# Kernel tuning notes

Measured on AMD Instinct MI355X. Metric: run time of the kernel, lower is better.

Reference implementation:

```python
import jax, jax.numpy as jnp
import numpy as np

B, TQ, TK, D, NA = 8, 512, 2048, 1024, 512
H, HD = 16, 64          # n_head, head_dim (D = H*HD)
NE, HID = 4, 32         # n_experts, expert hidden_dim
EPS = 1e-6


def _rmsnorm(x, w):
    return x * jax.lax.rsqrt(jnp.mean(x * x, axis=-1, keepdims=True) + EPS) * w


def setup_inputs() -> dict:
    key = jax.random.key(0)
    ks = jax.random.split(key, 20)
    r = lambda i, shp: jax.random.normal(ks[i], shp, dtype=jnp.float32) * 0.02
    return {
        'q': jax.random.normal(ks[0], (B, TQ, D), dtype=jnp.float32),
        'kv': jax.random.normal(ks[1], (B, TK, D), dtype=jnp.float32),
        'qn_w': jnp.ones((D,), jnp.float32),
        'kva_w': jnp.ones((D,), jnp.float32),
        'kvi_w': jnp.ones((D,), jnp.float32),
        'dn_w': jnp.ones((D,), jnp.float32),
        'fn_w': jnp.ones((D,), jnp.float32),
        'Wq': r(2, (D, D)), 'bq': jnp.zeros((D,), jnp.float32),
        'Wk': r(3, (D, D)), 'bk': jnp.zeros((D,), jnp.float32),
        'Wv': r(4, (D, D)), 'bv': jnp.zeros((D,), jnp.float32),
        'Wo': r(5, (D, D)), 'bo': jnp.zeros((D,), jnp.float32),
        'active_bias': r(6, (D,)),
        'inactive_bias': r(7, (D,)),
        'log_temp': jnp.array(0.0, jnp.float32),
        'gate_attn': jnp.array(0.3, jnp.float32),
        'gate_ffn': jnp.array(0.7, jnp.float32),
        'Wr': r(8, (D, NE)), 'br': jnp.zeros((NE,), jnp.float32),
        'W1': r(9, (NE, D, 2 * HID)), 'b1': jnp.zeros((NE, 2 * HID), jnp.float32),
        'W2': r(10, (NE, HID, D)), 'b2': jnp.zeros((NE, D), jnp.float32),
        'kv_mask': jnp.ones((B, TK), bool),
        'n_actives': NA,
    }


def _forward(q, kv, qn_w, kva_w, kvi_w, dn_w, fn_w,
             Wq, bq, Wk, bk, Wv, bv, Wo, bo,
             active_bias, inactive_bias, log_temp, gate_attn, gate_ffn,
             Wr, br, W1, b1, W2, b2, kv_mask, n_actives):
    Na = int(n_actives)
    Tk = kv.shape[1]
    Ni = Tk - Na
    b, tq, d = q.shape

    # split-normed kv, with active/inactive learned biases injected pre-KV-proj
    kv_a = _rmsnorm(kv[:, :Na], kva_w) + active_bias
    kv_i = _rmsnorm(kv[:, Na:], kvi_w) + inactive_bias
    kv_b = jnp.concatenate([kv_a, kv_i], axis=1)

    qn = _rmsnorm(q, qn_w)
    qp = (qn @ Wq + bq).reshape(b, tq, H, HD).transpose(0, 2, 1, 3)  # (B,H,Tq,hd)
    k = (kv_b @ Wk + bk).reshape(b, Tk, H, HD).transpose(0, 2, 1, 3)
    v = (kv_b @ Wv + bv).reshape(b, Tk, H, HD).transpose(0, 2, 1, 3)

    # torch: q *= 1/sqrt(hd), then SDPA(q/temp, ...) applies another 1/sqrt(hd)
    temp = jnp.clip(jnp.exp(log_temp), 0.1, 10.0)
    scale = 1.0 / (HD * temp)

    def attn(kk, vv):
        logits = jnp.einsum('bhqd,bhkd->bhqk', qp, kk) * scale
        return jnp.einsum('bhqk,bhkd->bhqd', jax.nn.softmax(logits, axis=-1), vv)

    out = attn(k[:, :, :Na], v[:, :, :Na]) / np.sqrt(max(Na, 1)) \
        - attn(k[:, :, Na:], v[:, :, Na:]) / np.sqrt(max(Ni, 1))
    out = out.transpose(0, 2, 1, 3).reshape(b, tq, d)
    delta = _rmsnorm(out @ Wo + bo, dn_w)
    q_new = q + jax.nn.sigmoid(gate_attn) * delta

    # dense soft MoE over normed kv, with query-similarity logit bias
    x = _rmsnorm(kv, fn_w)
    logits = x @ Wr + br                                   # (B,Tk,NE)
    q_vec = jnp.mean(q_new, axis=1, keepdims=True)         # (B,1,D)
    sim = jnp.einsum('bqd,btd->bt', q_vec, x)              # (B,Tk)
    probs = jax.nn.softmax(logits + sim[..., None], axis=-1)

    h = jnp.einsum('btd,edh->bteh', x, W1) + b1            # (B,Tk,NE,2*HID)
    xp, g = h[..., :HID], h[..., HID:]
    act = xp * (g * jax.nn.sigmoid(g))                     # SwiGLU
    eo = jnp.einsum('bteh,ehd->bted', act, W2) + b2        # (B,Tk,NE,D)
    moe_out = jnp.einsum('bte,bted->btd', probs, eo)

    kv_new = kv + jax.nn.sigmoid(gate_ffn) * moe_out
    return q_new, kv_new


def reference(q, kv, qn_w, kva_w, kvi_w, dn_w, fn_w,
              Wq, bq, Wk, bk, Wv, bv, Wo, bo,
              active_bias, inactive_bias, log_temp, gate_attn, gate_ffn,
              Wr, br, W1, b1, W2, b2, kv_mask, n_actives):
    return _forward(q, kv, qn_w, kva_w, kvi_w, dn_w, fn_w,
                    Wq, bq, Wk, bk, Wv, bv, Wo, bo,
                    active_bias, inactive_bias, log_temp, gate_attn, gate_ffn,
                    Wr, br, W1, b1, W2, b2, kv_mask, n_actives)
```

## Files before the change

### kernel.cpp

```cpp
#include <hip/hip_runtime.h>
#include <hip/hip_bf16.h>
#include <stdint.h>


#define B_   8
#define TQ_  512
#define TK_  2048
#define D_   1024
#define H_   16
#define HD_  64
#define NE_  4
#define HID_ 32
#define EPSF 1e-6f
#define LOG2E 1.44269504f

typedef __bf16 bf16_t;
typedef __bf16 bf16x8 __attribute__((ext_vector_type(8)));
typedef __bf16 bf16x4 __attribute__((ext_vector_type(4)));
typedef float  f32x4  __attribute__((ext_vector_type(4)));

typedef __attribute__((address_space(1))) void gvoid_t;
typedef __attribute__((address_space(3))) void lvoid_t;

__device__ __forceinline__ void gld_lds16(const void* g, void* l) {
  __builtin_amdgcn_global_load_lds((gvoid_t*)g, (lvoid_t*)l, 16, 0, 0);
}

struct TP4 { const float* in[4]; bf16_t* out[4]; };

__global__ void transpose_conv4_kernel(TP4 p) {
  __shared__ float tile[32][33];
  const int bz = blockIdx.z;
  const float* in = p.in[bz];
  bf16_t* out = p.out[bz];
  const int rb = blockIdx.y * 32, cb = blockIdx.x * 32;
  const int txi = threadIdx.x, tyi = threadIdx.y;
#pragma unroll
  for (int i = 0; i < 32; i += 8)
    tile[tyi + i][txi] = in[(size_t)(rb + tyi + i) * D_ + cb + txi];
  __syncthreads();
#pragma unroll
  for (int i = 0; i < 32; i += 8)
    out[(size_t)(cb + tyi + i) * D_ + rb + txi] = (bf16_t)tile[txi][tyi + i];
}

__global__ void transpose_conv_kernel(const float* __restrict__ in, bf16_t* __restrict__ out,
                                      int R, int C, int in_bstride,
                                      int out_rstride, int ob_row, int ob_col) {
  __shared__ float tile[32][33];
  const int bz = blockIdx.z;
  const int rb = blockIdx.y * 32, cb = blockIdx.x * 32;
  const int txi = threadIdx.x, tyi = threadIdx.y;
  const float* inp = in + (size_t)bz * in_bstride;
#pragma unroll
  for (int i = 0; i < 32; i += 8) {
    const int r = rb + tyi + i, c = cb + txi;
    if (r < R && c < C) tile[tyi + i][txi] = inp[(size_t)r * C + c];
  }
  __syncthreads();
#pragma unroll
  for (int i = 0; i < 32; i += 8) {
    const int orow = cb + tyi + i;
    const int ocol = rb + txi;
    if (orow < C && ocol < R)
      out[(size_t)(orow + bz * ob_row) * out_rstride + bz * ob_col + ocol] =
          (bf16_t)tile[txi][tyi + i];
  }
}

__device__ __forceinline__ float block_rsum(float v, float* red) {
  v += __shfl_xor(v, 1);  v += __shfl_xor(v, 2);  v += __shfl_xor(v, 4);
  v += __shfl_xor(v, 8);  v += __shfl_xor(v, 16); v += __shfl_xor(v, 32);
  const int tid = threadIdx.x;
  if ((tid & 63) == 0) red[tid >> 6] = v;
  __syncthreads();
  return red[0] + red[1] + red[2] + red[3];
}

__global__ __launch_bounds__(256)
void rms_kv_kernel(const float* __restrict__ kv, const float* __restrict__ kva_w,
                   const float* __restrict__ kvi_w, const float* __restrict__ fn_w,
                   const float* __restrict__ ab, const float* __restrict__ ib,
                   const int* __restrict__ n_act, const float* __restrict__ Wr,
                   const float* __restrict__ br,
                   bf16_t* __restrict__ kvb, bf16_t* __restrict__ xn,
                   float* __restrict__ probs) {
  __shared__ float red[4];
  __shared__ f32x4 pred[4];
  const int row = blockIdx.x;
  const int t = row & (TK_ - 1);
  const int tid = threadIdx.x;
  const float* src = kv + (size_t)row * D_;
  f32x4 v = ((const f32x4*)src)[tid];
  float ss = v[0]*v[0] + v[1]*v[1] + v[2]*v[2] + v[3]*v[3];
  ss = block_rsum(ss, red);
  const float rs = rsqrtf(ss * (1.0f / D_) + EPSF);
  const int Na = n_act[0];
  const float* wsel = (t < Na) ? kva_w : kvi_w;
  const float* bsel = (t < Na) ? ab : ib;
  const int d = tid * 4;
  f32x4 wv = *(const f32x4*)(wsel + d);
  f32x4 bv = *(const f32x4*)(bsel + d);
  f32x4 fv = *(const f32x4*)(fn_w + d);
  bf16x4 o0, o1;
  f32x4 p4 = {};
#pragma unroll
  for (int c = 0; c < 4; ++c) {
    const float xv = v[c] * rs;
    const float xf = xv * fv[c];
    o0[c] = (bf16_t)(xv * wv[c] + bv[c]);
    o1[c] = (bf16_t)xf;
    const f32x4 w4 = *(const f32x4*)&Wr[(d + c) * 4];
    p4 += w4 * xf;
  }
  *(bf16x4*)&kvb[(size_t)row * D_ + d] = o0;
  *(bf16x4*)&xn [(size_t)row * D_ + d] = o1;
#pragma unroll
  for (int m = 1; m <= 32; m <<= 1) {
    p4[0] += __shfl_xor(p4[0], m); p4[1] += __shfl_xor(p4[1], m);
    p4[2] += __shfl_xor(p4[2], m); p4[3] += __shfl_xor(p4[3], m);
  }
  if ((tid & 63) == 0) pred[tid >> 6] = p4;
  __syncthreads();
  if (tid == 0) {
    f32x4 s = pred[0] + pred[1] + pred[2] + pred[3];
    s[0] += br[0]; s[1] += br[1]; s[2] += br[2]; s[3] += br[3];
    const float mx = fmaxf(fmaxf(s[0], s[1]), fmaxf(s[2], s[3]));
    const float e0 = __expf(s[0] - mx), e1 = __expf(s[1] - mx);
    const float e2 = __expf(s[2] - mx), e3 = __expf(s[3] - mx);
    const float inv = 1.0f / (e0 + e1 + e2 + e3);
    f32x4 pr = { e0 * inv, e1 * inv, e2 * inv, e3 * inv };
    *(f32x4*)&probs[row * 4] = pr;
  }
}

__global__ __launch_bounds__(256)
void rms_q_kernel(const float* __restrict__ q, const float* __restrict__ qn_w,
                  bf16_t* __restrict__ qn) {
  __shared__ float red[4];
  const int row = blockIdx.x;
  const int tid = threadIdx.x;
  const float* src = q + (size_t)row * D_;
  f32x4 v = ((const f32x4*)src)[tid];
  float ss = v[0]*v[0] + v[1]*v[1] + v[2]*v[2] + v[3]*v[3];
  ss = block_rsum(ss, red);
  const float rs = rsqrtf(ss * (1.0f / D_) + EPSF);
  const int d = tid * 4;
  f32x4 wv = *(const f32x4*)(qn_w + d);
  bf16x4 o0;
#pragma unroll
  for (int c = 0; c < 4; ++c) o0[c] = (bf16_t)(v[c] * rs * wv[c]);
  *(bf16x4*)&qn[(size_t)row * D_ + d] = o0;
}

__device__ __forceinline__ int xcd_swz(int bx, int gx) {
  if ((gx & 7) == 0) { const int cpx = gx >> 3; return (bx & 7) * cpx + (bx >> 3); }
  return bx;
}

__device__ __forceinline__ void gemm_loop_db(const bf16_t* __restrict__ ga,
                                             const bf16_t* __restrict__ gb,
                                             bf16_t* As, bf16_t* Bs, int K,
                                             size_t rstep, int ar, int br2,
                                             int tid, f32x4 acc[4][4]) {
  gld_lds16(ga,         &As[tid * 8]);
  gld_lds16(ga + rstep, &As[2048 + tid * 8]);
  gld_lds16(gb,         &Bs[tid * 8]);
  gld_lds16(gb + rstep, &Bs[2048 + tid * 8]);
  int buf = 0;
  for (int k0 = 0; k0 < K; k0 += 32) {
    __syncthreads();
    if (k0 + 32 < K) {
      const int nb = buf ^ 1;
      gld_lds16(ga + k0 + 32,         &As[nb * 4096 + tid * 8]);
      gld_lds16(ga + k0 + 32 + rstep, &As[nb * 4096 + 2048 + tid * 8]);
      gld_lds16(gb + k0 + 32,         &Bs[nb * 4096 + tid * 8]);
      gld_lds16(gb + k0 + 32 + rstep, &Bs[nb * 4096 + 2048 + tid * 8]);
    }
    bf16x8 af[4], bfr[4];
#pragma unroll
    for (int i = 0; i < 4; ++i) af[i]  = *(const bf16x8*)&As[buf * 4096 + ar  + i * 512];
#pragma unroll
    for (int j = 0; j < 4; ++j) bfr[j] = *(const bf16x8*)&Bs[buf * 4096 + br2 + j * 512];
#pragma unroll
    for (int i = 0; i < 4; ++i)
#pragma unroll
      for (int j = 0; j < 4; ++j)
        acc[i][j] = __builtin_amdgcn_mfma_f32_16x16x32_bf16(af[i], bfr[j], acc[i][j], 0, 0, 0);
    buf ^= 1;
  }
}

__device__ __forceinline__ void gemm64_loop_db(const bf16_t* __restrict__ ga,
                                               const bf16_t* __restrict__ gb,
                                               bf16_t* As, bf16_t* Bs, int K,
                                               size_t rstep, int ar, int br2,
                                               int tid, f32x4 acc[2][4]) {
  gld_lds16(ga,         &As[tid * 8]);
  gld_lds16(gb,         &Bs[tid * 8]);
  gld_lds16(gb + rstep, &Bs[2048 + tid * 8]);
  int buf = 0;
  for (int k0 = 0; k0 < K; k0 += 32) {
    __syncthreads();
    if (k0 + 32 < K) {
      const int nb = buf ^ 1;
      gld_lds16(ga + k0 + 32,         &As[nb * 2048 + tid * 8]);
      gld_lds16(gb + k0 + 32,         &Bs[nb * 4096 + tid * 8]);
      gld_lds16(gb + k0 + 32 + rstep, &Bs[nb * 4096 + 2048 + tid * 8]);
    }
    bf16x8 af[2], bfr[4];
#pragma unroll
    for (int i = 0; i < 2; ++i) af[i]  = *(const bf16x8*)&As[buf * 2048 + ar  + i * 512];
#pragma unroll
    for (int j = 0; j < 4; ++j) bfr[j] = *(const bf16x8*)&Bs[buf * 4096 + br2 + j * 512];
#pragma unroll
    for (int i = 0; i < 2; ++i)
#pragma unroll
      for (int j = 0; j < 4; ++j)
        acc[i][j] = __builtin_amdgcn_mfma_f32_16x16x32_bf16(af[i], bfr[j], acc[i][j], 0, 0, 0);
    buf ^= 1;
  }
}

template<int HAS_BIAS>
__global__ __launch_bounds__(256)
void gemm_tn(const bf16_t* __restrict__ A, const bf16_t* __restrict__ Wt,
             const float* __restrict__ bias, bf16_t* __restrict__ C,
             int M, int N, int K) {
  __shared__ alignas(16) bf16_t As[2 * 128 * 32];
  __shared__ alignas(16) bf16_t Bs[2 * 128 * 32];
  const int tid = threadIdx.x;
  const int lane = tid & 63;
  const int w = tid >> 6;
  const int wr = w >> 1, wc = w & 1;
  const int m0 = xcd_swz(blockIdx.x, gridDim.x) * 128;
  const int n0 = blockIdx.y * 128;

  f32x4 acc[4][4] = {};
  const bf16_t* ga = A  + (size_t)(m0 + (tid >> 2)) * K + (tid & 3) * 8;
  const bf16_t* gb = Wt + (size_t)(n0 + (tid >> 2)) * K + (tid & 3) * 8;
  const int kb = (lane >> 4) * 8;
  const int ar  = ((wr * 64 + (lane & 15)) << 5) + kb;
  const int br2 = ((wc * 64 + (lane & 15)) << 5) + kb;

  gemm_loop_db(ga, gb, As, Bs, K, (size_t)64 * K, ar, br2, tid, acc);

  const int row0 = m0 + wr * 64 + ((lane >> 4) << 2);
  const int col0 = n0 + wc * 64 + (lane & 15);
#pragma unroll
  for (int j = 0; j < 4; ++j) {
    const int cc = col0 + j * 16;
    const float bv = HAS_BIAS ? bias[cc] : 0.0f;
#pragma unroll
    for (int i = 0; i < 4; ++i) {
      const int rr = row0 + i * 16;
#pragma unroll
      for (int r = 0; r < 4; ++r)
        C[(size_t)(rr + r) * N + cc] = (bf16_t)(acc[i][j][r] + bv);
    }
  }
}

template<int HAS_BIAS>
__global__ __launch_bounds__(256)
void gemm64_tn(const bf16_t* __restrict__ A, const bf16_t* __restrict__ Wt,
               const float* __restrict__ bias, bf16_t* __restrict__ C,
               int M, int N, int K) {
  __shared__ alignas(16) bf16_t As[2 * 64 * 32];
  __shared__ alignas(16) bf16_t Bs[2 * 128 * 32];
  const int tid = threadIdx.x;
  const int lane = tid & 63;
  const int w = tid >> 6;
  const int wr = w >> 1, wc = w & 1;
  const int m0 = xcd_swz(blockIdx.x, gridDim.x) * 64;
  const int n0 = blockIdx.y * 128;

  f32x4 acc[2][4] = {};
  const bf16_t* ga = A  + (size_t)(m0 + (tid >> 2)) * K + (tid & 3) * 8;
  const bf16_t* gb = Wt + (size_t)(n0 + (tid >> 2)) * K + (tid & 3) * 8;
  const int kb = (lane >> 4) * 8;
  const int ar  = ((wr * 32 + (lane & 15)) << 5) + kb;
  const int br2 = ((wc * 64 + (lane & 15)) << 5) + kb;

  gemm64_loop_db(ga, gb, As, Bs, K, (size_t)64 * K, ar, br2, tid, acc);

  const int row0 = m0 + wr * 32 + ((lane >> 4) << 2);
  const int col0 = n0 + wc * 64 + (lane & 15);
#pragma unroll
  for (int j = 0; j < 4; ++j) {
    const int cc = col0 + j * 16;
    const float bv = HAS_BIAS ? bias[cc] : 0.0f;
#pragma unroll
    for (int i = 0; i < 2; ++i) {
      const int rr = row0 + i * 16;
#pragma unroll
      for (int r = 0; r < 4; ++r)
        C[(size_t)(rr + r) * N + cc] = (bf16_t)(acc[i][j][r] + bv);
    }
  }
}

__global__ __launch_bounds__(256)
void gemm_vt(const bf16_t* __restrict__ A, const bf16_t* __restrict__ Wt0,
             const float* __restrict__ bias, bf16_t* __restrict__ C0) {
  __shared__ alignas(16) bf16_t As[2 * 128 * 32];
  __shared__ alignas(16) bf16_t Bs[2 * 128 * 32];
  const int K = D_, N = TK_;
  const bf16_t* Wt = Wt0 + (size_t)blockIdx.z * TK_ * D_;
  bf16_t* C = C0 + (size_t)blockIdx.z * D_ * TK_;
  const int tid = threadIdx.x;
  const int lane = tid & 63;
  const int w = tid >> 6;
  const int wr = w >> 1, wc = w & 1;
  const int m0 = blockIdx.x * 128;
  const int n0 = blockIdx.y * 128;

  f32x4 acc[4][4] = {};
  const bf16_t* ga = A  + (size_t)(m0 + (tid >> 2)) * K + (tid & 3) * 8;
  const bf16_t* gb = Wt + (size_t)(n0 + (tid >> 2)) * K + (tid & 3) * 8;
  const int kb = (lane >> 4) * 8;
  const int ar  = ((wr * 64 + (lane & 15)) << 5) + kb;
  const int br2 = ((wc * 64 + (lane & 15)) << 5) + kb;

  gemm_loop_db(ga, gb, As, Bs, K, (size_t)64 * K, ar, br2, tid, acc);

  const int row0 = m0 + wr * 64 + ((lane >> 4) << 2);
  const int col0 = n0 + wc * 64 + (lane & 15);
#pragma unroll
  for (int i = 0; i < 4; ++i) {
    const int rr = row0 + i * 16;
#pragma unroll
    for (int r = 0; r < 4; ++r) {
      const float bv = bias[rr + r];
#pragma unroll
      for (int j = 0; j < 4; ++j)
        C[(size_t)(rr + r) * N + col0 + j * 16] = (bf16_t)(acc[i][j][r] + bv);
    }
  }
}

__global__ __launch_bounds__(256)
void gemm64_h_act(const bf16_t* __restrict__ A, const bf16_t* __restrict__ Wt,
                  const float* __restrict__ bias, const float* __restrict__ probs,
                  bf16_t* __restrict__ a2) {
  __shared__ alignas(16) bf16_t As[2 * 64 * 32];
  __shared__ alignas(16) bf16_t Bs[2 * 128 * 32];
  const int K = D_;
  const int tid = threadIdx.x;
  const int lane = tid & 63;
  const int w = tid >> 6;
  const int wr = w >> 1, wc = w & 1;
  const int m0 = xcd_swz(blockIdx.x, gridDim.x) * 64;
  const int n0 = blockIdx.y * 128;

  f32x4 acc[2][4] = {};
  const bf16_t* ga = A  + (size_t)(m0 + (tid >> 2)) * K + (tid & 3) * 8;
  const bf16_t* gb = Wt + (size_t)(n0 + (tid >> 2)) * K + (tid & 3) * 8;
  const int kb = (lane >> 4) * 8;
  const int ar  = ((wr * 32 + (lane & 15)) << 5) + kb;
  const int br2 = ((wc * 64 + (lane & 15)) << 5) + kb;

  gemm64_loop_db(ga, gb, As, Bs, K, (size_t)64 * K, ar, br2, tid, acc);

  const int row0 = m0 + wr * 32 + ((lane >> 4) << 2);
  const int hbase = n0 + wc * 64 + (lane & 15);
  const int e = hbase >> 6;
#pragma unroll
  for (int j = 0; j < 2; ++j) {
    const int ch = hbase + j * 16;
    const float bx = bias[ch], bg = bias[ch + 32];
    const int ac = (ch & 63) + e * 32;
#pragma unroll
    for (int i = 0; i < 2; ++i) {
      const int rr = row0 + i * 16;
#pragma unroll
      for (int r = 0; r < 4; ++r) {
        const float xp = acc[i][j][r] + bx;
        const float g  = acc[i][j + 2][r] + bg;
        const float sg = 1.0f / (1.0f + __expf(-g));
        const float pr = probs[(size_t)(rr + r) * 4 + e];
        a2[(size_t)(rr + r) * 128 + ac] = (bf16_t)(pr * xp * g * sg);
      }
    }
  }
}

__global__ __launch_bounds__(256)
void gemm_moe_kvnew(const bf16_t* __restrict__ A, const bf16_t* __restrict__ Wt,
                    const float* __restrict__ kv, const float* __restrict__ probs,
                    const float* __restrict__ b2, const float* __restrict__ gate_ffn,
                    float* __restrict__ out) {
  __shared__ alignas(16) bf16_t As[2 * 128 * 32];
  __shared__ alignas(16) bf16_t Bs[2 * 128 * 32];
  const int K = 128, N = D_;
  const int tid = threadIdx.x;
  const int lane = tid & 63;
  const int w = tid >> 6;
  const int wr = w >> 1, wc = w & 1;
  const int m0 = xcd_swz(blockIdx.x, gridDim.x) * 128;
  const int n0 = blockIdx.y * 128;

  f32x4 acc[4][4] = {};
  const bf16_t* ga = A  + (size_t)(m0 + (tid >> 2)) * K + (tid & 3) * 8;
  const bf16_t* gb = Wt + (size_t)(n0 + (tid >> 2)) * K + (tid & 3) * 8;
  const int kb = (lane >> 4) * 8;
  const int ar  = ((wr * 64 + (lane & 15)) << 5) + kb;
  const int br2 = ((wc * 64 + (lane & 15)) << 5) + kb;

  gemm_loop_db(ga, gb, As, Bs, K, (size_t)64 * K, ar, br2, tid, acc);

  const float sgf = 1.0f / (1.0f + __expf(-gate_ffn[0]));
  const int row0 = m0 + wr * 64 + ((lane >> 4) << 2);
  const int col0 = n0 + wc * 64 + (lane & 15);
#pragma unroll
  for (int j = 0; j < 4; ++j) {
    const int cc = col0 + j * 16;
    const f32x4 b2v = { b2[0 * D_ + cc], b2[1 * D_ + cc], b2[2 * D_ + cc], b2[3 * D_ + cc] };
#pragma unroll
    for (int i = 0; i < 4; ++i) {
      const int rr = row0 + i * 16;
#pragma unroll
      for (int r = 0; r < 4; ++r) {
        const f32x4 pr = *(const f32x4*)&probs[(size_t)(rr + r) * 4];
        const float bsum = pr[0]*b2v[0] + pr[1]*b2v[1] + pr[2]*b2v[2] + pr[3]*b2v[3];
        out[(size_t)(rr + r) * N + cc] =
            kv[(size_t)(rr + r) * N + cc] + sgf * (acc[i][j][r] + bsum);
      }
    }
  }
}

__global__ __launch_bounds__(256, 3)
void attn_mfma_kernel(const bf16_t* __restrict__ qp, const bf16_t* __restrict__ kb,
                      const bf16_t* __restrict__ vt, bf16_t* __restrict__ attno,
                      const float* __restrict__ log_temp, const int* __restrict__ n_act) {
  __shared__ alignas(16) bf16_t Ks[2][64 * 64];
  __shared__ alignas(16) bf16_t Vs[2][64 * 64];
  __shared__ alignas(16) bf16_t Ps[4][32 * 64];

  const int dd = blockIdx.x;
  const int xcd = dd & 7, within = dd >> 3;
  const int qt = within & 3, slot0 = within >> 2;
  const int bh = slot0 * 8 + xcd;
  const int b = bh >> 4, h = bh & 15;

  const int tid = threadIdx.x;
  const int lane = tid & 63;
  const int w = tid >> 6;
  const int lane15 = lane & 15, lgrp = lane >> 4, l7 = lane & 7;
  const int Na = n_act[0];
  float temp = __expf(log_temp[0]);
  temp = fminf(fmaxf(temp, 0.1f), 10.0f);
  const float lsc = LOG2E / (64.0f * temp);
  const int rowbase = qt * 128 + w * 32;

  const bf16_t* qsrcA = qp + (size_t)(b * TQ_ + rowbase + lane15) * D_ + h * 64 + lgrp * 8;
  const bf16_t* qsrcB = qsrcA + (size_t)16 * D_;
  bf16x8 qfA0 = *(const bf16x8*)qsrcA;
  bf16x8 qfA1 = *(const bf16x8*)(qsrcA + 32);
  bf16x8 qfB0 = *(const bf16x8*)qsrcB;
  bf16x8 qfB1 = *(const bf16x8*)(qsrcB + 32);
#pragma unroll
  for (int j = 0; j < 8; ++j) {
    qfA0[j] = (bf16_t)((float)qfA0[j] * lsc);
    qfA1[j] = (bf16_t)((float)qfA1[j] * lsc);
    qfB0[j] = (bf16_t)((float)qfB0[j] * lsc);
    qfB1[j] = (bf16_t)((float)qfB1[j] * lsc);
  }

  const int srow = tid >> 3;
  const int schunk = (tid & 7) ^ (srow & 7);
  const bf16_t* ksrc = kb + (size_t)(b * TK_ + srow) * D_ + h * 64 + schunk * 8;
  const bf16_t* vsrc = vt + ((size_t)(b * 16 + h) * 64 + srow) * TK_ + schunk * 8;

  f32x4 oA[4] = {}, oB[4] = {}, outA[4] = {}, outB[4] = {};
  float laccA = 0.f, laccB = 0.f;

  const float inv_sa = rsqrtf((float)(Na > 1 ? Na : 1));
  const int Ni = TK_ - Na;
  const float inv_si = rsqrtf((float)(Ni > 1 ? Ni : 1));

  gld_lds16(ksrc,            &Ks[0][tid * 8]);
  gld_lds16(ksrc + 32 * D_,  &Ks[0][2048 + tid * 8]);
  gld_lds16(vsrc,            &Vs[0][tid * 8]);
  gld_lds16(vsrc + 32 * TK_, &Vs[0][2048 + tid * 8]);

  for (int t = 0; t < TK_ / 64; ++t) {
    const int cur = t & 1;
    __syncthreads();
    if (t + 1 < TK_ / 64) {
      const int nb = cur ^ 1;
      const bf16_t* kN = ksrc + (size_t)(t + 1) * 64 * D_;
      const bf16_t* vN = vsrc + (size_t)(t + 1) * 64;
      gld_lds16(kN,            &Ks[nb][tid * 8]);
      gld_lds16(kN + 32 * D_,  &Ks[nb][2048 + tid * 8]);
      gld_lds16(vN,            &Vs[nb][tid * 8]);
      gld_lds16(vN + 32 * TK_, &Vs[nb][2048 + tid * 8]);
    }

    f32x4 sA[4], sB[4];
    __builtin_amdgcn_s_setprio(1);
#pragma unroll
    for (int cf = 0; cf < 4; ++cf) {
      const int krow = (cf * 16 + lane15) * 64;
      const bf16x8 kf0 = *(const bf16x8*)&Ks[cur][krow + ((lgrp ^ l7) << 3)];
      const bf16x8 kf1 = *(const bf16x8*)&Ks[cur][krow + (((lgrp + 4) ^ l7) << 3)];
      f32x4 s = {};
      s = __builtin_amdgcn_mfma_f32_16x16x32_bf16(kf0, qfA0, s, 0, 0, 0);
      s = __builtin_amdgcn_mfma_f32_16x16x32_bf16(kf1, qfA1, s, 0, 0, 0);
      sA[cf] = s;
      f32x4 s2 = {};
      s2 = __builtin_amdgcn_mfma_f32_16x16x32_bf16(kf0, qfB0, s2, 0, 0, 0);
      s2 = __builtin_amdgcn_mfma_f32_16x16x32_bf16(kf1, qfB1, s2, 0, 0, 0);
      sB[cf] = s2;
    }
    __builtin_amdgcn_s_setprio(0);

#pragma unroll
    for (int cf = 0; cf < 4; ++cf) {
      const int c = cf * 2 + (lgrp >> 1);
      const int pcol = ((c ^ l7) << 3) + (lgrp & 1) * 4;
      f32x4 pA, pB;
#pragma unroll
      for (int r = 0; r < 4; ++r) pA[r] = exp2f(sA[cf][r]);
#pragma unroll
      for (int r = 0; r < 4; ++r) pB[r] = exp2f(sB[cf][r]);
      laccA += (pA[0] + pA[1]) + (pA[2] + pA[3]);
      laccB += (pB[0] + pB[1]) + (pB[2] + pB[3]);
      bf16x4 pvA, pvB;
#pragma unroll
      for (int r = 0; r < 4; ++r) { pvA[r] = (bf16_t)pA[r]; pvB[r] = (bf16_t)pB[r]; }
      *(bf16x4*)&Ps[w][lane15 * 64 + pcol]        = pvA;
      *(bf16x4*)&Ps[w][(16 + lane15) * 64 + pcol] = pvB;
    }

    {
      const int prowA = lane15 * 64;
      const int prowB = (16 + lane15) * 64;
      const bf16x8 paA0 = *(const bf16x8*)&Ps[w][prowA + ((lgrp ^ l7) << 3)];
      const bf16x8 paA1 = *(const bf16x8*)&Ps[w][prowA + (((lgrp + 4) ^ l7) << 3)];
      const bf16x8 paB0 = *(const bf16x8*)&Ps[w][prowB + ((lgrp ^ l7) << 3)];
      const bf16x8 paB1 = *(const bf16x8*)&Ps[w][prowB + (((lgrp + 4) ^ l7) << 3)];
      __builtin_amdgcn_s_setprio(1);
#pragma unroll
      for (int df = 0; df < 4; ++df) {
        const int vrow = (df * 16 + lane15) * 64;
        const bf16x8 vf0 = *(const bf16x8*)&Vs[cur][vrow + ((lgrp ^ l7) << 3)];
        const bf16x8 vf1 = *(const bf16x8*)&Vs[cur][vrow + (((lgrp + 4) ^ l7) << 3)];
        oA[df] = __builtin_amdgcn_mfma_f32_16x16x32_bf16(paA0, vf0, oA[df], 0, 0, 0);
        oA[df] = __builtin_amdgcn_mfma_f32_16x16x32_bf16(paA1, vf1, oA[df], 0, 0, 0);
        oB[df] = __builtin_amdgcn_mfma_f32_16x16x32_bf16(paB0, vf0, oB[df], 0, 0, 0);
        oB[df] = __builtin_amdgcn_mfma_f32_16x16x32_bf16(paB1, vf1, oB[df], 0, 0, 0);
      }
      __builtin_amdgcn_s_setprio(0);
    }

    const bool endA = ((t + 1) * 64 == Na);
    const bool endI = (t == TK_ / 64 - 1);
    if (endA || endI) {
      float lA = laccA, lB = laccB;
      lA += __shfl_xor(lA, 16); lA += __shfl_xor(lA, 32);
      lB += __shfl_xor(lB, 16); lB += __shfl_xor(lB, 32);
      const float ssc = endA ? inv_sa : -inv_si;
      f32x4 ivA, ivB;
#pragma unroll
      for (int r = 0; r < 4; ++r) {
        ivA[r] = ssc / __shfl(lA, lgrp * 4 + r);
        ivB[r] = ssc / __shfl(lB, lgrp * 4 + r);
      }
#pragma unroll
      for (int df = 0; df < 4; ++df) {
        outA[df] += oA[df] * ivA; oA[df] = (f32x4){};
        outB[df] += oB[df] * ivB; oB[df] = (f32x4){};
      }
      laccA = 0.f; laccB = 0.f;
    }
  }

#pragma unroll
  for (int df = 0; df < 4; ++df)
#pragma unroll
    for (int r = 0; r < 4; ++r) {
      const size_t ro = (size_t)(b * TQ_ + rowbase + lgrp * 4 + r) * D_ + h * 64 + df * 16 + lane15;
      attno[ro]             = (bf16_t)outA[df][r];
      attno[ro + 16 * D_]   = (bf16_t)outB[df][r];
    }
}

__global__ __launch_bounds__(256)
void delta_qnew_kernel(const bf16_t* __restrict__ proj, const float* __restrict__ dn_w,
                       const float* __restrict__ q, const float* __restrict__ gate_attn,
                       float* __restrict__ qnew) {
  __shared__ float red[4];
  const int row = blockIdx.x;
  const int tid = threadIdx.x;
  bf16x4 pv = *(const bf16x4*)(proj + (size_t)row * D_ + tid * 4);
  f32x4 v;
#pragma unroll
  for (int c = 0; c < 4; ++c) v[c] = (float)pv[c];
  float ss = v[0]*v[0] + v[1]*v[1] + v[2]*v[2] + v[3]*v[3];
  ss = block_rsum(ss, red);
  const float rs = rsqrtf(ss * (1.0f / D_) + EPSF);
  const float sga = 1.0f / (1.0f + __expf(-gate_attn[0]));
  const int d = tid * 4;
  f32x4 wv = *(const f32x4*)(dn_w + d);
  f32x4 qv = *(const f32x4*)(q + (size_t)row * D_ + d);
  f32x4 out;
#pragma unroll
  for (int c = 0; c < 4; ++c) out[c] = qv[c] + sga * (v[c] * rs * wv[c]);
  *(f32x4*)&qnew[(size_t)row * D_ + d] = out;
}

extern "C" void kernel_launch(void* const* d_in, const int* in_sizes, int n_in,
                              void* d_out, int out_size, void* d_ws, size_t ws_size,
                              hipStream_t stream) {
  const float* q           = (const float*)d_in[0];
  const float* kv          = (const float*)d_in[1];
  const float* qn_w        = (const float*)d_in[2];
  const float* kva_w       = (const float*)d_in[3];
  const float* kvi_w       = (const float*)d_in[4];
  const float* dn_w        = (const float*)d_in[5];
  const float* fn_w        = (const float*)d_in[6];
  const float* Wq          = (const float*)d_in[7];
  const float* bq          = (const float*)d_in[8];
  const float* Wk          = (const float*)d_in[9];
  const float* bk          = (const float*)d_in[10];
  const float* Wv          = (const float*)d_in[11];
  const float* bv          = (const float*)d_in[12];
  const float* Wo          = (const float*)d_in[13];
  const float* bo          = (const float*)d_in[14];
  const float* active_bias = (const float*)d_in[15];
  const float* inactive_b  = (const float*)d_in[16];
  const float* log_temp    = (const float*)d_in[17];
  const float* gate_attn   = (const float*)d_in[18];
  const float* gate_ffn    = (const float*)d_in[19];
  const float* Wr          = (const float*)d_in[20];
  const float* br          = (const float*)d_in[21];
  const float* W1          = (const float*)d_in[22];
  const float* b1          = (const float*)d_in[23];
  const float* W2          = (const float*)d_in[24];
  const float* b2          = (const float*)d_in[25];
  const int*   n_act       = (const int*)d_in[27];

  char* ws = (char*)d_ws;
  size_t off = 0;
  auto alloc = [&](size_t bytes) -> char* {
    char* p = ws + off;
    off = (off + bytes + 255) & ~(size_t)255;
    return p;
  };

  bf16_t* wqT  = (bf16_t*)alloc((size_t)D_ * D_ * 2);
  bf16_t* wkT  = (bf16_t*)alloc((size_t)D_ * D_ * 2);
  bf16_t* wvT  = (bf16_t*)alloc((size_t)D_ * D_ * 2);
  bf16_t* woT  = (bf16_t*)alloc((size_t)D_ * D_ * 2);
  bf16_t* w1T  = (bf16_t*)alloc((size_t)256 * D_ * 2);
  bf16_t* w2T  = (bf16_t*)alloc((size_t)D_ * 128 * 2);
  bf16_t* kvb  = (bf16_t*)alloc((size_t)B_ * TK_ * D_ * 2);
  bf16_t* xn   = (bf16_t*)alloc((size_t)B_ * TK_ * D_ * 2);
  bf16_t* qn   = (bf16_t*)alloc((size_t)B_ * TQ_ * D_ * 2);
  bf16_t* qp   = (bf16_t*)alloc((size_t)B_ * TQ_ * D_ * 2);
  bf16_t* kbuf = (bf16_t*)alloc((size_t)B_ * TK_ * D_ * 2);
  bf16_t* vt   = (bf16_t*)alloc((size_t)B_ * D_ * TK_ * 2);
  float*  probs = (float*)alloc((size_t)B_ * TK_ * NE_ * 4);
  bf16_t* attno = qn;
  bf16_t* proj  = qp;
  bf16_t* a2buf = kbuf;
  (void)ws_size; (void)in_sizes; (void)n_in; (void)out_size;

  float* q_new_out  = (float*)d_out;
  float* kv_new_out = (float*)d_out + (size_t)B_ * TQ_ * D_;

  dim3 tb(32, 8);
  TP4 tp;
  tp.in[0] = Wq; tp.in[1] = Wk; tp.in[2] = Wv; tp.in[3] = Wo;
  tp.out[0] = wqT; tp.out[1] = wkT; tp.out[2] = wvT; tp.out[3] = woT;
  transpose_conv4_kernel<<<dim3(32, 32, 4), tb, 0, stream>>>(tp);
  transpose_conv_kernel<<<dim3(2, 32, 4), tb, 0, stream>>>(W1, w1T, D_, 64, D_ * 64, D_, 64, 0);
  transpose_conv_kernel<<<dim3(32, 1, 4), tb, 0, stream>>>(W2, w2T, 32, D_, 32 * D_, 128, 0, 32);

  rms_kv_kernel<<<B_ * TK_, 256, 0, stream>>>(kv, kva_w, kvi_w, fn_w, active_bias,
                                              inactive_b, n_act, Wr, br, kvb, xn, probs);
  rms_q_kernel<<<B_ * TQ_, 256, 0, stream>>>(q, qn_w, qn);

  gemm64_tn<1><<<dim3(B_ * TQ_ / 64, D_ / 128), 256, 0, stream>>>(qn, wqT, bq, qp, B_ * TQ_, D_, D_);
  gemm_tn<1><<<dim3(B_ * TK_ / 128, D_ / 128), 256, 0, stream>>>(kvb, wkT, bk, kbuf, B_ * TK_, D_, D_);
  gemm_vt<<<dim3(D_ / 128, TK_ / 128, B_), 256, 0, stream>>>(wvT, kvb, bv, vt);

  attn_mfma_kernel<<<B_ * H_ * (TQ_ / 128), 256, 0, stream>>>(qp, kbuf, vt, attno, log_temp, n_act);

  gemm64_tn<1><<<dim3(B_ * TQ_ / 64, D_ / 128), 256, 0, stream>>>(attno, woT, bo, proj, B_ * TQ_, D_, D_);
  delta_qnew_kernel<<<B_ * TQ_, 256, 0, stream>>>(proj, dn_w, q, gate_attn, q_new_out);

  gemm64_h_act<<<dim3(B_ * TK_ / 64, 2), 256, 0, stream>>>(xn, w1T, b1, probs, a2buf);
  gemm_moe_kvnew<<<dim3(B_ * TK_ / 128, D_ / 128), 256, 0, stream>>>(a2buf, w2T, kv, probs, b2,
                                                                     gate_ffn, kv_new_out);
}
```

Baseline: 339.4 us.

## Fuse K and V projections into one GEMM and halve attention block size

Merges the K projection and the transposed V projection into a single kernel that loads each kv tile once and drives two MFMA accumulator sets. The V result is transposed through LDS so it can be written to the Vt layout with coalesced stores. This removes one launch and one full read of the normalized kv activations, at the cost of more accumulator registers and extra LDS traffic in the epilogue. The attention kernel is also reconfigured to 128-thread blocks covering 64 query rows, which doubles the grid and changes the K/V tile loading pattern.

```diff
diff --git a/kernel.cpp b/kernel.cpp
--- a/kernel.cpp
+++ b/kernel.cpp
@@ -156,6 +156,111 @@
 __device__ __forceinline__ int xcd_swz(int bx, int gx) {
   if ((gx & 7) == 0) { const int cpx = gx >> 3; return (bx & 7) * cpx + (bx >> 3); }
   return bx;
+}
+
+__global__ __launch_bounds__(256)
+void gemm_kv(const bf16_t* __restrict__ A, const bf16_t* __restrict__ Wk,
+             const bf16_t* __restrict__ Wv, const float* __restrict__ bk,
+             const float* __restrict__ bv, bf16_t* __restrict__ Kout,
+             bf16_t* __restrict__ Vt) {
+  __shared__ alignas(16) bf16_t lds[3 * 8192];
+  bf16_t* As  = lds;
+  bf16_t* Bks = lds + 8192;
+  bf16_t* Bvs = lds + 16384;
+  const int K = D_;
+  const int tid = threadIdx.x;
+  const int lane = tid & 63;
+  const int w = tid >> 6;
+  const int wr = w >> 1, wc = w & 1;
+  const int lane15 = lane & 15, lgrp = lane >> 4;
+  const int m0 = xcd_swz(blockIdx.x, gridDim.x) * 128;
+  const int n0 = blockIdx.y * 128;
+
+  f32x4 acc_k[4][4] = {};
+  f32x4 acc_v[4][4] = {};
+
+  const bf16_t* ga = A  + (size_t)(m0 + (tid >> 2)) * K + (tid & 3) * 8;
+  const bf16_t* gk = Wk + (size_t)(n0 + (tid >> 2)) * K + (tid & 3) * 8;
+  const bf16_t* gv = Wv + (size_t)(n0 + (tid >> 2)) * K + (tid & 3) * 8;
+  const size_t rstep = (size_t)64 * K;
+  const int kb = lgrp * 8;
+  const int ar  = ((wr * 64 + lane15) << 5) + kb;
+  const int br2 = ((wc * 64 + lane15) << 5) + kb;
+
+  gld_lds16(ga,         &As[tid * 8]);
+  gld_lds16(ga + rstep, &As[2048 + tid * 8]);
+  gld_lds16(gk,         &Bks[tid * 8]);
+  gld_lds16(gk + rstep, &Bks[2048 + tid * 8]);
+  gld_lds16(gv,         &Bvs[tid * 8]);
+  gld_lds16(gv + rstep, &Bvs[2048 + tid * 8]);
+  int buf = 0;
+  for (int k0 = 0; k0 < K; k0 += 32) {
+    __syncthreads();
+    if (k0 + 32 < K) {
+      const int nb = buf ^ 1;
+      gld_lds16(ga + k0 + 32,         &As[nb * 4096 + tid * 8]);
+      gld_lds16(ga + k0 + 32 + rstep, &As[nb * 4096 + 2048 + tid * 8]);
+      gld_lds16(gk + k0 + 32,         &Bks[nb * 4096 + tid * 8]);
+      gld_lds16(gk + k0 + 32 + rstep, &Bks[nb * 4096 + 2048 + tid * 8]);
+      gld_lds16(gv + k0 + 32,         &Bvs[nb * 4096 + tid * 8]);
+      gld_lds16(gv + k0 + 32 + rstep, &Bvs[nb * 4096 + 2048 + tid * 8]);
+    }
+    bf16x8 af[4], bkf[4], bvf[4];
+#pragma unroll
+    for (int i = 0; i < 4; ++i) af[i]  = *(const bf16x8*)&As [buf * 4096 + ar  + i * 512];
+#pragma unroll
+    for (int j = 0; j < 4; ++j) bkf[j] = *(const bf16x8*)&Bks[buf * 4096 + br2 + j * 512];
+#pragma unroll
+    for (int j = 0; j < 4; ++j) bvf[j] = *(const bf16x8*)&Bvs[buf * 4096 + br2 + j * 512];
+    __builtin_amdgcn_s_setprio(1);
+#pragma unroll
+    for (int i = 0; i < 4; ++i)
+#pragma unroll
+      for (int j = 0; j < 4; ++j) {
+        acc_k[i][j] = __builtin_amdgcn_mfma_f32_16x16x32_bf16(af[i], bkf[j], acc_k[i][j], 0, 0, 0);
+        acc_v[i][j] = __builtin_amdgcn_mfma_f32_16x16x32_bf16(af[i], bvf[j], acc_v[i][j], 0, 0, 0);
+      }
+    __builtin_amdgcn_s_setprio(0);
+    buf ^= 1;
+  }
+
+  const int row0 = m0 + wr * 64 + (lgrp << 2);
+  const int col0 = n0 + wc * 64 + lane15;
+#pragma unroll
+  for (int j = 0; j < 4; ++j) {
+    const int cc = col0 + j * 16;
+    const float bkv = bk[cc];
+#pragma unroll
+    for (int i = 0; i < 4; ++i) {
+      const int rr = row0 + i * 16;
+#pragma unroll
+      for (int r = 0; r < 4; ++r)
+        Kout[(size_t)(rr + r) * D_ + cc] = (bf16_t)(acc_k[i][j][r] + bkv);
+    }
+  }
+
+  __syncthreads();
+  bf16_t* vt_l = lds + w * 4608;
+#pragma unroll
+  for (int j = 0; j < 4; ++j) {
+    const int nl = j * 16 + lane15;
+    const float bvv = bv[n0 + wc * 64 + nl];
+#pragma unroll
+    for (int i = 0; i < 4; ++i)
+#pragma unroll
+      for (int r = 0; r < 4; ++r)
+        vt_l[nl * 72 + i * 16 + lgrp * 4 + r] = (bf16_t)(acc_v[i][j][r] + bvv);
+  }
+  const int bidx2 = m0 >> 11;
+  const int tok0 = (m0 & (TK_ - 1)) + wr * 64;
+  bf16_t* vbase = Vt + (size_t)bidx2 * D_ * TK_ + (size_t)(n0 + wc * 64) * TK_ + tok0;
+#pragma unroll
+  for (int it = 0; it < 8; ++it) {
+    const int ln = (lane >> 3) + it * 8;
+    const int tk = (lane & 7) * 8;
+    const bf16x8 v8 = *(const bf16x8*)&vt_l[ln * 72 + tk];
+    *(bf16x8*)&vbase[(size_t)ln * TK_ + tk] = v8;
+  }
 }
 
 __device__ __forceinline__ void gemm_loop_db(const bf16_t* __restrict__ ga,
@@ -224,45 +329,6 @@
 
 template<int HAS_BIAS>
 __global__ __launch_bounds__(256)
-void gemm_tn(const bf16_t* __restrict__ A, const bf16_t* __restrict__ Wt,
-             const float* __restrict__ bias, bf16_t* __restrict__ C,
-             int M, int N, int K) {
-  __shared__ alignas(16) bf16_t As[2 * 128 * 32];
-  __shared__ alignas(16) bf16_t Bs[2 * 128 * 32];
-  const int tid = threadIdx.x;
-  const int lane = tid & 63;
-  const int w = tid >> 6;
-  const int wr = w >> 1, wc = w & 1;
-  const int m0 = xcd_swz(blockIdx.x, gridDim.x) * 128;
-  const int n0 = blockIdx.y * 128;
-
-  f32x4 acc[4][4] = {};
-  const bf16_t* ga = A  + (size_t)(m0 + (tid >> 2)) * K + (tid & 3) * 8;
-  const bf16_t* gb = Wt + (size_t)(n0 + (tid >> 2)) * K + (tid & 3) * 8;
-  const int kb = (lane >> 4) * 8;
-  const int ar  = ((wr * 64 + (lane & 15)) << 5) + kb;
-  const int br2 = ((wc * 64 + (lane & 15)) << 5) + kb;
-
-  gemm_loop_db(ga, gb, As, Bs, K, (size_t)64 * K, ar, br2, tid, acc);
-
-  const int row0 = m0 + wr * 64 + ((lane >> 4) << 2);
-  const int col0 = n0 + wc * 64 + (lane & 15);
-#pragma unroll
-  for (int j = 0; j < 4; ++j) {
-    const int cc = col0 + j * 16;
-    const float bv = HAS_BIAS ? bias[cc] : 0.0f;
-#pragma unroll
-    for (int i = 0; i < 4; ++i) {
-      const int rr = row0 + i * 16;
-#pragma unroll
-      for (int r = 0; r < 4; ++r)
-        C[(size_t)(rr + r) * N + cc] = (bf16_t)(acc[i][j][r] + bv);
-    }
-  }
-}
-
-template<int HAS_BIAS>
-__global__ __launch_bounds__(256)
 void gemm64_tn(const bf16_t* __restrict__ A, const bf16_t* __restrict__ Wt,
                const float* __restrict__ bias, bf16_t* __restrict__ C,
                int M, int N, int K) {
@@ -296,45 +362,6 @@
 #pragma unroll
       for (int r = 0; r < 4; ++r)
         C[(size_t)(rr + r) * N + cc] = (bf16_t)(acc[i][j][r] + bv);
-    }
-  }
-}
-
-__global__ __launch_bounds__(256)
-void gemm_vt(const bf16_t* __restrict__ A, const bf16_t* __restrict__ Wt0,
-             const float* __restrict__ bias, bf16_t* __restrict__ C0) {
-  __shared__ alignas(16) bf16_t As[2 * 128 * 32];
-  __shared__ alignas(16) bf16_t Bs[2 * 128 * 32];
-  const int K = D_, N = TK_;
-  const bf16_t* Wt = Wt0 + (size_t)blockIdx.z * TK_ * D_;
-  bf16_t* C = C0 + (size_t)blockIdx.z * D_ * TK_;
-  const int tid = threadIdx.x;
-  const int lane = tid & 63;
-  const int w = tid >> 6;
-  const int wr = w >> 1, wc = w & 1;
-  const int m0 = blockIdx.x * 128;
-  const int n0 = blockIdx.y * 128;
-
-  f32x4 acc[4][4] = {};
-  const bf16_t* ga = A  + (size_t)(m0 + (tid >> 2)) * K + (tid & 3) * 8;
-  const bf16_t* gb = Wt + (size_t)(n0 + (tid >> 2)) * K + (tid & 3) * 8;
-  const int kb = (lane >> 4) * 8;
-  const int ar  = ((wr * 64 + (lane & 15)) << 5) + kb;
-  const int br2 = ((wc * 64 + (lane & 15)) << 5) + kb;
-
-  gemm_loop_db(ga, gb, As, Bs, K, (size_t)64 * K, ar, br2, tid, acc);
-
-  const int row0 = m0 + wr * 64 + ((lane >> 4) << 2);
-  const int col0 = n0 + wc * 64 + (lane & 15);
-#pragma unroll
-  for (int i = 0; i < 4; ++i) {
-    const int rr = row0 + i * 16;
-#pragma unroll
-    for (int r = 0; r < 4; ++r) {
-      const float bv = bias[rr + r];
-#pragma unroll
-      for (int j = 0; j < 4; ++j)
-        C[(size_t)(rr + r) * N + col0 + j * 16] = (bf16_t)(acc[i][j][r] + bv);
     }
   }
 }
@@ -430,17 +457,17 @@
   }
 }
 
-__global__ __launch_bounds__(256, 3)
+__global__ __launch_bounds__(128, 2)
 void attn_mfma_kernel(const bf16_t* __restrict__ qp, const bf16_t* __restrict__ kb,
                       const bf16_t* __restrict__ vt, bf16_t* __restrict__ attno,
                       const float* __restrict__ log_temp, const int* __restrict__ n_act) {
   __shared__ alignas(16) bf16_t Ks[2][64 * 64];
   __shared__ alignas(16) bf16_t Vs[2][64 * 64];
-  __shared__ alignas(16) bf16_t Ps[4][32 * 64];
+  __shared__ alignas(16) bf16_t Ps[2][32 * 64];
 
   const int dd = blockIdx.x;
   const int xcd = dd & 7, within = dd >> 3;
-  const int qt = within & 3, slot0 = within >> 2;
+  const int qt = within & 7, slot0 = within >> 3;
   const int bh = slot0 * 8 + xcd;
   const int b = bh >> 4, h = bh & 15;
 
@@ -452,7 +479,7 @@
   float temp = __expf(log_temp[0]);
   temp = fminf(fmaxf(temp, 0.1f), 10.0f);
   const float lsc = LOG2E / (64.0f * temp);
-  const int rowbase = qt * 128 + w * 32;
+  const int rowbase = qt * 64 + w * 32;
 
   const bf16_t* qsrcA = qp + (size_t)(b * TQ_ + rowbase + lane15) * D_ + h * 64 + lgrp * 8;
   const bf16_t* qsrcB = qsrcA + (size_t)16 * D_;
@@ -480,10 +507,11 @@
   const int Ni = TK_ - Na;
   const float inv_si = rsqrtf((float)(Ni > 1 ? Ni : 1));
 
-  gld_lds16(ksrc,            &Ks[0][tid * 8]);
-  gld_lds16(ksrc + 32 * D_,  &Ks[0][2048 + tid * 8]);
-  gld_lds16(vsrc,            &Vs[0][tid * 8]);
-  gld_lds16(vsrc + 32 * TK_, &Vs[0][2048 + tid * 8]);
+#pragma unroll
+  for (int r = 0; r < 4; ++r) {
+    gld_lds16(ksrc + (size_t)r * 16 * D_, &Ks[0][r * 1024 + tid * 8]);
+    gld_lds16(vsrc + (size_t)r * 16 * TK_, &Vs[0][r * 1024 + tid * 8]);
+  }
 
   for (int t = 0; t < TK_ / 64; ++t) {
     const int cur = t & 1;
@@ -492,10 +520,11 @@
       const int nb = cur ^ 1;
       const bf16_t* kN = ksrc + (size_t)(t + 1) * 64 * D_;
       const bf16_t* vN = vsrc + (size_t)(t + 1) * 64;
-      gld_lds16(kN,            &Ks[nb][tid * 8]);
-      gld_lds16(kN + 32 * D_,  &Ks[nb][2048 + tid * 8]);
-      gld_lds16(vN,            &Vs[nb][tid * 8]);
-      gld_lds16(vN + 32 * TK_, &Vs[nb][2048 + tid * 8]);
+#pragma unroll
+      for (int r = 0; r < 4; ++r) {
+        gld_lds16(kN + (size_t)r * 16 * D_, &Ks[nb][r * 1024 + tid * 8]);
+        gld_lds16(vN + (size_t)r * 16 * TK_, &Vs[nb][r * 1024 + tid * 8]);
+      }
     }
 
     f32x4 sA[4], sB[4];
@@ -582,8 +611,8 @@
 #pragma unroll
     for (int r = 0; r < 4; ++r) {
       const size_t ro = (size_t)(b * TQ_ + rowbase + lgrp * 4 + r) * D_ + h * 64 + df * 16 + lane15;
-      attno[ro]             = (bf16_t)outA[df][r];
-      attno[ro + 16 * D_]   = (bf16_t)outB[df][r];
+      attno[ro]           = (bf16_t)outA[df][r];
+      attno[ro + 16 * D_] = (bf16_t)outB[df][r];
     }
 }
 
@@ -684,10 +713,9 @@
   rms_q_kernel<<<B_ * TQ_, 256, 0, stream>>>(q, qn_w, qn);
 
   gemm64_tn<1><<<dim3(B_ * TQ_ / 64, D_ / 128), 256, 0, stream>>>(qn, wqT, bq, qp, B_ * TQ_, D_, D_);
-  gemm_tn<1><<<dim3(B_ * TK_ / 128, D_ / 128), 256, 0, stream>>>(kvb, wkT, bk, kbuf, B_ * TK_, D_, D_);
-  gemm_vt<<<dim3(D_ / 128, TK_ / 128, B_), 256, 0, stream>>>(wvT, kvb, bv, vt);
-
-  attn_mfma_kernel<<<B_ * H_ * (TQ_ / 128), 256, 0, stream>>>(qp, kbuf, vt, attno, log_temp, n_act);
+  gemm_kv<<<dim3(B_ * TK_ / 128, D_ / 128), 256, 0, stream>>>(kvb, wkT, wvT, bk, bv, kbuf, vt);
+
+  attn_mfma_kernel<<<B_ * H_ * (TQ_ / 64), 128, 0, stream>>>(qp, kbuf, vt, attno, log_temp, n_act);
 
   gemm64_tn<1><<<dim3(B_ * TQ_ / 64, D_ / 128), 256, 0, stream>>>(attno, woT, bo, proj, B_ * TQ_, D_, D_);
   delta_qnew_kernel<<<B_ * TQ_, 256, 0, stream>>>(proj, dn_w, q, gate_attn, q_new_out);
```

Result: no change. 342.1 us (+0.8%).
